# Kernel tuning notes

Hardware: AMD Instinct MI355X
Metric: run time of the kernel (lower is better)

## Reference

```python
import jax, jax.numpy as jnp
import numpy as np

DIM = 768
NUM_HEADS = 12
WH, WW = 14, 14
N_TOK = WH * WW + 1  # 197, includes CLS token
NUM_REL_DIST = (2 * WH - 1) * (2 * WW - 1) + 3  # 732
HEAD_DIM = DIM // NUM_HEADS
SCALE = HEAD_DIM ** -0.5


def _relative_position_index():
    # Mirrors the torch buffer construction (constant, int).
    coords = np.stack(np.meshgrid(np.arange(WH), np.arange(WW), indexing='ij'))  # [2,WH,WW]
    cf = coords.reshape(2, -1)  # [2, WH*WW]
    rel = cf[:, :, None] - cf[:, None, :]  # [2, N, N]
    rel = rel.transpose(1, 2, 0).astype(np.int64)
    rel[:, :, 0] += WH - 1
    rel[:, :, 1] += WW - 1
    rel[:, :, 0] *= 2 * WW - 1
    idx = np.zeros((N_TOK, N_TOK), dtype=np.int64)
    idx[1:, 1:] = rel.sum(-1)
    idx[0, 0:] = NUM_REL_DIST - 3
    idx[0:, 0] = NUM_REL_DIST - 2
    idx[0, 0] = NUM_REL_DIST - 1
    return jnp.asarray(idx)

REL_POS_INDEX = _relative_position_index()


def setup_inputs() -> dict:
    key = jax.random.key(0)
    ks = jax.random.split(key, 7)
    B = 64
    x = jax.random.normal(ks[0], (B, N_TOK, DIM), dtype=jnp.float32)
    qkv_weight = jax.random.normal(ks[1], (3 * DIM, DIM), dtype=jnp.float32) * 0.02
    q_bias = jax.random.normal(ks[2], (DIM,), dtype=jnp.float32) * 0.02
    v_bias = jax.random.normal(ks[3], (DIM,), dtype=jnp.float32) * 0.02
    rel_pos_bias_table = jax.random.normal(ks[4], (NUM_REL_DIST, NUM_HEADS), dtype=jnp.float32) * 0.02
    proj_weight = jax.random.normal(ks[5], (DIM, DIM), dtype=jnp.float32) * 0.02
    proj_bias = jax.random.normal(ks[6], (DIM,), dtype=jnp.float32) * 0.02
    return {"x": x, "qkv_weight": qkv_weight, "q_bias": q_bias, "v_bias": v_bias,
            "rel_pos_bias_table": rel_pos_bias_table, "proj_weight": proj_weight,
            "proj_bias": proj_bias}


def reference(x, qkv_weight, q_bias, v_bias, rel_pos_bias_table, proj_weight, proj_bias):
    B, N, C = x.shape
    qkv_bias = jnp.concatenate([q_bias, jnp.zeros_like(v_bias), v_bias])
    qkv = x @ qkv_weight.T + qkv_bias  # [B, N, 3C]
    qkv = qkv.reshape(B, N, 3, NUM_HEADS, HEAD_DIM).transpose(2, 0, 3, 1, 4)
    q, k, v = qkv[0], qkv[1], qkv[2]  # each [B, H, N, D]
    attn = jnp.einsum('bhnd,bhmd->bhnm', q * SCALE, k)  # [B, H, N, N]
    rpb = rel_pos_bias_table[REL_POS_INDEX]  # [N, N, H]
    attn = attn + rpb.transpose(2, 0, 1)[None]  # [1, H, N, N]
    attn = jax.nn.softmax(attn, axis=-1)
    out = jnp.einsum('bhnm,bhmd->bhnd', attn, v)  # [B, H, N, D]
    out = out.transpose(0, 2, 1, 3).reshape(B, N, C)
    return out @ proj_weight.T + proj_bias
```

## Files before the change

### kernel.cpp

```cpp
#include <hip/hip_runtime.h>
#include <hip/hip_bf16.h>

#define DIM 768
#define NHEADS 12
#define NTOK 197
#define NP 208
#define NPS 232
#define M_ROWS 12608
#define M_PAD 12672
#define HEADS_TOT 768

typedef __attribute__((ext_vector_type(8))) short bf16x8;
typedef __attribute__((ext_vector_type(4))) float f32x4;

__device__ inline short f2bf(float f) {
  union { __hip_bfloat16 h; short s; } u;
  u.h = __float2bfloat16(f);
  return u.s;
}

__device__ __forceinline__ void gload16(const short* g, short* l) {
  __builtin_amdgcn_global_load_lds((const __attribute__((address_space(1))) void*)g,
                                   (__attribute__((address_space(3))) void*)l, 16, 0, 0);
}

__device__ __forceinline__ int xcd_swz(int orig, int nwg) {
  int q = nwg >> 3, r = nwg & 7;
  int x = orig & 7, p = orig >> 3;
  return (x < r ? x * (q + 1) : r * (q + 1) + (x - r) * q) + p;
}

__global__ void convert_kernel(const float* __restrict__ x, const float* __restrict__ wq,
                               const float* __restrict__ wp,
                               short* __restrict__ xb, short* __restrict__ wqb,
                               short* __restrict__ wpb) {
  int idx = blockIdx.x * 256 + threadIdx.x;
  const int n_x  = M_ROWS * DIM / 4;
  const int n_wq = 3 * DIM * DIM / 4;
  const int n_wp = DIM * DIM / 4;
  const float4* src; short* dst; int off;
  if (idx < n_x)                { src = (const float4*)x;  dst = xb;  off = idx; }
  else if (idx < n_x + n_wq)    { src = (const float4*)wq; dst = wqb; off = idx - n_x; }
  else if (idx < n_x + n_wq + n_wp) { src = (const float4*)wp; dst = wpb; off = idx - n_x - n_wq; }
  else return;
  float4 v = src[off];
  short4 o;
  o.x = f2bf(v.x); o.y = f2bf(v.y); o.z = f2bf(v.z); o.w = f2bf(v.w);
  *(short4*)(dst + (size_t)off * 4) = o;
}

__global__ void rpb_kernel(const float* __restrict__ table, float* __restrict__ rpbf) {
  int idx = blockIdx.x * 256 + threadIdx.x;
  const int tot = NHEADS * NP * NP;
  if (idx >= tot) return;
  int h = idx / (NP * NP);
  int rem = idx - h * NP * NP;
  int i = rem / NP;
  int j = rem - i * NP;
  float v = 0.f;
  if (i < NTOK && j < NTOK) {
    int t;
    if (i == 0 && j == 0) t = 731;
    else if (i == 0)      t = 729;
    else if (j == 0)      t = 730;
    else {
      int p = i - 1, q = j - 1;
      int ri = p / 14, ci = p - ri * 14;
      int rj = q / 14, cj = q - rj * 14;
      t = (ri - rj + 13) * 27 + (ci - cj + 13);
    }
    v = table[t * NHEADS + h];
  }
  rpbf[idx] = v;
}

__device__ inline void gemm_tile_mainloop(const short* __restrict__ A, const short* __restrict__ Bw,
                                          int tm, int tn,
                                          short* As0, short* Bs0, short* As1, short* Bs1,
                                          f32x4 (&acc)[4][4]) {
  const int tid = threadIdx.x;
  const int l = tid & 63, lr = l & 15, lg = l >> 4;
  const int w = tid >> 6, wm = w >> 1, wn = w & 1;
  const int row = tid >> 2;
  const int c8 = (((tid & 3) ^ ((tid >> 3) & 3)) << 3);
  const int rs = (((lg ^ ((lr >> 1) & 3))) << 3);
  const short* Ag = A + (size_t)(tm * 128 + row) * DIM + c8;
  const short* Bg = Bw + (size_t)(tn * 128 + row) * DIM + c8;
  const int dOff = tid * 8;
#pragma unroll
  for (int m = 0; m < 4; ++m)
#pragma unroll
    for (int n = 0; n < 4; ++n) { f32x4 z = {0.f, 0.f, 0.f, 0.f}; acc[m][n] = z; }

  gload16(Ag, As0 + dOff);
  gload16(Ag + (size_t)64 * DIM, As0 + 2048 + dOff);
  gload16(Bg, Bs0 + dOff);
  gload16(Bg + (size_t)64 * DIM, Bs0 + 2048 + dOff);
  __syncthreads();

  const int NT = DIM / 32;
  for (int kt = 0; kt < NT; ++kt) {
    short* Ac = (kt & 1) ? As1 : As0;
    short* Bc = (kt & 1) ? Bs1 : Bs0;
    short* An = (kt & 1) ? As0 : As1;
    short* Bn = (kt & 1) ? Bs0 : Bs1;
    if (kt < NT - 1) {
      gload16(Ag + (kt + 1) * 32, An + dOff);
      gload16(Ag + (size_t)64 * DIM + (kt + 1) * 32, An + 2048 + dOff);
      gload16(Bg + (kt + 1) * 32, Bn + dOff);
      gload16(Bg + (size_t)64 * DIM + (kt + 1) * 32, Bn + 2048 + dOff);
    }
    bf16x8 af[4], bfr[4];
#pragma unroll
    for (int m = 0; m < 4; ++m)
      af[m] = *(const bf16x8*)(Ac + (wm * 64 + m * 16 + lr) * 32 + rs);
#pragma unroll
    for (int n = 0; n < 4; ++n)
      bfr[n] = *(const bf16x8*)(Bc + (wn * 64 + n * 16 + lr) * 32 + rs);
#pragma unroll
    for (int m = 0; m < 4; ++m)
#pragma unroll
      for (int n = 0; n < 4; ++n)
        acc[m][n] = __builtin_amdgcn_mfma_f32_16x16x32_bf16(af[m], bfr[n], acc[m][n], 0, 0, 0);
    __syncthreads();
  }
}

__global__ void gemm_qkv_kernel(const short* __restrict__ xb, const short* __restrict__ wqb,
                                const float* __restrict__ q_bias, const float* __restrict__ v_bias,
                                short* __restrict__ qbuf, short* __restrict__ kbuf,
                                short* __restrict__ vtbuf) {
  __shared__ __attribute__((aligned(16))) short As0[128 * 32];
  __shared__ __attribute__((aligned(16))) short Bs0[128 * 32];
  __shared__ __attribute__((aligned(16))) short As1[128 * 32];
  __shared__ __attribute__((aligned(16))) short Bs1[128 * 32];
  const int wg = xcd_swz(blockIdx.x, 99 * 18);
  const int tn = wg % 18, tm = wg / 18;
  f32x4 acc[4][4];
  gemm_tile_mainloop(xb, wqb, tm, tn, As0, Bs0, As1, Bs1, acc);

  const int tid = threadIdx.x;
  const int w = tid >> 6, l = tid & 63, lr = l & 15, lg = l >> 4;
  const int wm = w >> 1, wn = w & 1;
  const int rbase = tm * 128 + wm * 64, cbase = tn * 128 + wn * 64;
#pragma unroll
  for (int n = 0; n < 4; ++n) {
    int c = cbase + n * 16 + lr;
    int part = (c < 768) ? 0 : ((c < 1536) ? 1 : 2);
    int f = c - part * 768;
    int hh = f >> 6, d = f & 63;
    float bias = (part == 0) ? q_bias[c] : ((part == 2) ? v_bias[f] : 0.f);
#pragma unroll
    for (int m = 0; m < 4; ++m) {
#pragma unroll
      for (int i = 0; i < 4; ++i) {
        int r = rbase + m * 16 + lg * 4 + i;
        if (r < M_ROWS) {
          int b = r / 197, nn = r - b * 197;
          int bh = b * 12 + hh;
          float v = acc[m][n][i] + bias;
          if (part == 0)      qbuf[(size_t)(bh * NP + nn) * 64 + d] = f2bf(v * 0.125f);
          else if (part == 1) kbuf[(size_t)(bh * NP + nn) * 64 + d] = f2bf(v);
          else                vtbuf[(size_t)(bh * 64 + d) * NP + nn] = f2bf(v);
        }
      }
    }
  }
}

__global__ __launch_bounds__(512, 1)
void attn_kernel(const short* __restrict__ qbuf, const short* __restrict__ kbuf,
                 const short* __restrict__ vtbuf, const float* __restrict__ rpbf,
                 short* __restrict__ aout) {
  __shared__ __attribute__((aligned(16))) short Klds[208 * 64];
  __shared__ __attribute__((aligned(16))) short Vlds[64 * NPS];
  __shared__ __attribute__((aligned(16))) short Plds[8 * 16 * NPS];
  const int bh = blockIdx.x;
  const int b = bh / 12, h = bh - b * 12;
  const short* Qg = qbuf + (size_t)bh * NP * 64;
  const short* Kg = kbuf + (size_t)bh * NP * 64;
  const short* Vg = vtbuf + (size_t)bh * 64 * NP;
  const float* RP = rpbf + (size_t)h * NP * NP;
  const int tid = threadIdx.x;
  const int wave = tid >> 6, l = tid & 63, lr = l & 15, lg = l >> 4;

  for (int c = tid; c < 1664; c += 512) {
    int r = c >> 3, sp = c & 7;
    gload16(Kg + r * 64 + ((sp ^ (r & 7)) << 3), Klds + c * 8);
  }
  for (int c = tid; c < 64 * 29; c += 512) {
    int r = c / 29, sp = c - r * 29;
    int sg = sp < 26 ? sp : 25;
    gload16(Vg + r * NP + sg * 8, Vlds + c * 8);
  }
  __syncthreads();
  if (tid < 64) {
    for (int j = NTOK; j < NPS; ++j) Vlds[tid * NPS + j] = 0;
  }
  __syncthreads();

  short* Pw = Plds + wave * 16 * NPS;
  for (int s = wave; s < 13; s += 8) {
    const int row0 = s * 16;
    bf16x8 qf0 = *(const bf16x8*)(Qg + (row0 + lr) * 64 + lg * 8);
    bf16x8 qf1 = *(const bf16x8*)(Qg + (row0 + lr) * 64 + 32 + lg * 8);
    f32x4 acc[13];
#pragma unroll
    for (int t = 0; t < 13; ++t) { f32x4 z = {0.f, 0.f, 0.f, 0.f}; acc[t] = z; }
    __builtin_amdgcn_s_setprio(1);
#pragma unroll
    for (int t = 0; t < 13; ++t) {
      int rk = t * 16 + lr;
      int sw = lr & 7;
      bf16x8 kf0 = *(const bf16x8*)(Klds + rk * 64 + ((lg ^ sw) << 3));
      bf16x8 kf1 = *(const bf16x8*)(Klds + rk * 64 + (((4 + lg) ^ sw) << 3));
      acc[t] = __builtin_amdgcn_mfma_f32_16x16x32_bf16(qf0, kf0, acc[t], 0, 0, 0);
      acc[t] = __builtin_amdgcn_mfma_f32_16x16x32_bf16(qf1, kf1, acc[t], 0, 0, 0);
    }
    __builtin_amdgcn_s_setprio(0);
    float sum4[4];
#pragma unroll
    for (int i = 0; i < 4; ++i) {
      const int row = row0 + lg * 4 + i;
      const float* rp = RP + (size_t)row * NP;
      float sv[13];
      float mx = -3e38f;
#pragma unroll
      for (int t = 0; t < 13; ++t) {
        int col = t * 16 + lr;
        float s_ = (col < NTOK) ? (acc[t][i] + rp[col]) : -3e38f;
        sv[t] = s_;
        mx = fmaxf(mx, s_);
      }
      mx = fmaxf(mx, __shfl_xor(mx, 1, 16));
      mx = fmaxf(mx, __shfl_xor(mx, 2, 16));
      mx = fmaxf(mx, __shfl_xor(mx, 4, 16));
      mx = fmaxf(mx, __shfl_xor(mx, 8, 16));
      float sm = 0.f;
#pragma unroll
      for (int t = 0; t < 13; ++t) {
        float p = __expf(sv[t] - mx);
        sm += p;
        Pw[(lg * 4 + i) * NPS + t * 16 + lr] = f2bf(p);
      }
      sm += __shfl_xor(sm, 1, 16);
      sm += __shfl_xor(sm, 2, 16);
      sm += __shfl_xor(sm, 4, 16);
      sm += __shfl_xor(sm, 8, 16);
      sum4[i] = sm;
      Pw[(lg * 4 + i) * NPS + 208 + lr] = 0;
    }
    f32x4 o[4];
#pragma unroll
    for (int dt = 0; dt < 4; ++dt) { f32x4 z = {0.f, 0.f, 0.f, 0.f}; o[dt] = z; }
    __builtin_amdgcn_s_setprio(1);
#pragma unroll
    for (int jb = 0; jb < 7; ++jb) {
      bf16x8 pf = *(const bf16x8*)(Pw + lr * NPS + jb * 32 + lg * 8);
#pragma unroll
      for (int dt = 0; dt < 4; ++dt) {
        bf16x8 vf = *(const bf16x8*)(Vlds + (dt * 16 + lr) * NPS + jb * 32 + lg * 8);
        o[dt] = __builtin_amdgcn_mfma_f32_16x16x32_bf16(pf, vf, o[dt], 0, 0, 0);
      }
    }
    __builtin_amdgcn_s_setprio(0);
#pragma unroll
    for (int i = 0; i < 4; ++i) {
      const int row = row0 + lg * 4 + i;
      if (row < NTOK) {
        float inv = 1.f / sum4[i];
        size_t base = (size_t)(b * 197 + row) * DIM + h * 64;
#pragma unroll
        for (int dt = 0; dt < 4; ++dt)
          aout[base + dt * 16 + lr] = f2bf(o[dt][i] * inv);
      }
    }
  }
}

__global__ void gemm_proj_kernel(const short* __restrict__ ab, const short* __restrict__ wpb,
                                 const float* __restrict__ proj_bias, float* __restrict__ out) {
  __shared__ __attribute__((aligned(16))) short As0[128 * 32];
  __shared__ __attribute__((aligned(16))) short Bs0[128 * 32];
  __shared__ __attribute__((aligned(16))) short As1[128 * 32];
  __shared__ __attribute__((aligned(16))) short Bs1[128 * 32];
  const int wg = xcd_swz(blockIdx.x, 99 * 6);
  const int tn = wg % 6, tm = wg / 6;
  f32x4 acc[4][4];
  gemm_tile_mainloop(ab, wpb, tm, tn, As0, Bs0, As1, Bs1, acc);

  const int tid = threadIdx.x;
  const int w = tid >> 6, l = tid & 63, lr = l & 15, lg = l >> 4;
  const int wm = w >> 1, wn = w & 1;
  const int rbase = tm * 128 + wm * 64, cbase = tn * 128 + wn * 64;
#pragma unroll
  for (int n = 0; n < 4; ++n) {
    int c = cbase + n * 16 + lr;
    float pb = proj_bias[c];
#pragma unroll
    for (int m = 0; m < 4; ++m) {
#pragma unroll
      for (int i = 0; i < 4; ++i) {
        int r = rbase + m * 16 + lg * 4 + i;
        if (r < M_ROWS) out[(size_t)r * DIM + c] = acc[m][n][i] + pb;
      }
    }
  }
}

extern "C" void kernel_launch(void* const* d_in, const int* in_sizes, int n_in,
                              void* d_out, int out_size, void* d_ws, size_t ws_size,
                              hipStream_t stream) {
  const float* x         = (const float*)d_in[0];
  const float* wqkv      = (const float*)d_in[1];
  const float* q_bias    = (const float*)d_in[2];
  const float* v_bias    = (const float*)d_in[3];
  const float* table     = (const float*)d_in[4];
  const float* wproj     = (const float*)d_in[5];
  const float* proj_bias = (const float*)d_in[6];
  float* out = (float*)d_out;

  char* p = (char*)d_ws;
  short* xb    = (short*)p; p += (size_t)M_PAD * DIM * 2;
  short* wqb   = (short*)p; p += (size_t)3 * DIM * DIM * 2;
  short* wpb   = (short*)p; p += (size_t)DIM * DIM * 2;
  short* qbuf  = (short*)p; p += (size_t)HEADS_TOT * NP * 64 * 2;
  short* kbuf  = (short*)p; p += (size_t)HEADS_TOT * NP * 64 * 2;
  short* vtbuf = (short*)p; p += (size_t)HEADS_TOT * 64 * NP * 2;
  float* rpbf  = (float*)p; p += (size_t)NHEADS * NP * NP * 4;
  short* aout  = xb;

  const int conv_tot = (M_ROWS * DIM + 3 * DIM * DIM + DIM * DIM) / 4;
  convert_kernel<<<(conv_tot + 255) / 256, 256, 0, stream>>>(x, wqkv, wproj, xb, wqb, wpb);
  rpb_kernel<<<(NHEADS * NP * NP + 255) / 256, 256, 0, stream>>>(table, rpbf);
  gemm_qkv_kernel<<<99 * 18, 256, 0, stream>>>(xb, wqb, q_bias, v_bias, qbuf, kbuf, vtbuf);
  attn_kernel<<<HEADS_TOT, 512, 0, stream>>>(qbuf, kbuf, vtbuf, rpbf, aout);
  gemm_proj_kernel<<<99 * 6, 256, 0, stream>>>(aout, wpb, proj_bias, out);
}
```

Before: 173.6 us.

## Store QKV as row-major token buffer and gather per-head in attention

The QKV GEMM epilogue now writes a plain row-major [M, 2304] bf16 buffer instead of scattering into per-head Q/K and transposed V buffers, which removes the per-element division and the strided transposed V stores. The attention kernel then reads Q, K and V with a 2304-element row stride, clamping padded rows. V is transposed into LDS with scalar 2-byte loads instead of the 16-byte async copies used before. The input padding grows to 12800 rows and is zeroed in the convert kernel so the extra GEMM tile row reads defined data. The cost moves from scattered global writes in the GEMM to uncoalesced scalar V reads in attention.

```diff
diff --git a/kernel.cpp b/kernel.cpp
--- a/kernel.cpp
+++ b/kernel.cpp
@@ -2,13 +2,15 @@
 #include <hip/hip_bf16.h>
 
 #define DIM 768
+#define QKVD 2304
 #define NHEADS 12
 #define NTOK 197
 #define NP 208
 #define NPS 232
 #define M_ROWS 12608
-#define M_PAD 12672
+#define M_PAD 12800
 #define HEADS_TOT 768
+#define NT 24
 
 typedef __attribute__((ext_vector_type(8))) short bf16x8;
 typedef __attribute__((ext_vector_type(4))) float f32x4;
@@ -38,11 +40,19 @@
   const int n_x  = M_ROWS * DIM / 4;
   const int n_wq = 3 * DIM * DIM / 4;
   const int n_wp = DIM * DIM / 4;
+  const int n_pad = (M_PAD - M_ROWS) * DIM / 4;
+  if (idx >= n_x + n_wq + n_wp) {
+    int k = idx - n_x - n_wq - n_wp;
+    if (k < n_pad) {
+      short4 z = {0, 0, 0, 0};
+      *(short4*)(xb + (size_t)M_ROWS * DIM + (size_t)k * 4) = z;
+    }
+    return;
+  }
   const float4* src; short* dst; int off;
-  if (idx < n_x)                { src = (const float4*)x;  dst = xb;  off = idx; }
-  else if (idx < n_x + n_wq)    { src = (const float4*)wq; dst = wqb; off = idx - n_x; }
-  else if (idx < n_x + n_wq + n_wp) { src = (const float4*)wp; dst = wpb; off = idx - n_x - n_wq; }
-  else return;
+  if (idx < n_x)             { src = (const float4*)x;  dst = xb;  off = idx; }
+  else if (idx < n_x + n_wq) { src = (const float4*)wq; dst = wqb; off = idx - n_x; }
+  else                       { src = (const float4*)wp; dst = wpb; off = idx - n_x - n_wq; }
   float4 v = src[off];
   short4 o;
   o.x = f2bf(v.x); o.y = f2bf(v.y); o.z = f2bf(v.z); o.w = f2bf(v.w);
@@ -74,10 +84,10 @@
   rpbf[idx] = v;
 }
 
-__device__ inline void gemm_tile_mainloop(const short* __restrict__ A, const short* __restrict__ Bw,
-                                          int tm, int tn,
-                                          short* As0, short* Bs0, short* As1, short* Bs1,
-                                          f32x4 (&acc)[4][4]) {
+__device__ inline void gemm_tile_mainloop128(const short* __restrict__ A, const short* __restrict__ Bw,
+                                             int tm, int tn,
+                                             short* As0, short* Bs0, short* As1, short* Bs1,
+                                             f32x4 (&acc)[4][4]) {
   const int tid = threadIdx.x;
   const int l = tid & 63, lr = l & 15, lg = l >> 4;
   const int w = tid >> 6, wm = w >> 1, wn = w & 1;
@@ -98,7 +108,6 @@
   gload16(Bg + (size_t)64 * DIM, Bs0 + 2048 + dOff);
   __syncthreads();
 
-  const int NT = DIM / 32;
   for (int kt = 0; kt < NT; ++kt) {
     short* Ac = (kt & 1) ? As1 : As0;
     short* Bc = (kt & 1) ? Bs1 : Bs0;
@@ -128,16 +137,15 @@
 
 __global__ void gemm_qkv_kernel(const short* __restrict__ xb, const short* __restrict__ wqb,
                                 const float* __restrict__ q_bias, const float* __restrict__ v_bias,
-                                short* __restrict__ qbuf, short* __restrict__ kbuf,
-                                short* __restrict__ vtbuf) {
+                                short* __restrict__ qkvb) {
   __shared__ __attribute__((aligned(16))) short As0[128 * 32];
   __shared__ __attribute__((aligned(16))) short Bs0[128 * 32];
   __shared__ __attribute__((aligned(16))) short As1[128 * 32];
   __shared__ __attribute__((aligned(16))) short Bs1[128 * 32];
-  const int wg = xcd_swz(blockIdx.x, 99 * 18);
+  const int wg = xcd_swz(blockIdx.x, 100 * 18);
   const int tn = wg % 18, tm = wg / 18;
   f32x4 acc[4][4];
-  gemm_tile_mainloop(xb, wqb, tm, tn, As0, Bs0, As1, Bs1, acc);
+  gemm_tile_mainloop128(xb, wqb, tm, tn, As0, Bs0, As1, Bs1, acc);
 
   const int tid = threadIdx.x;
   const int w = tid >> 6, l = tid & 63, lr = l & 15, lg = l >> 4;
@@ -147,63 +155,57 @@
   for (int n = 0; n < 4; ++n) {
     int c = cbase + n * 16 + lr;
     int part = (c < 768) ? 0 : ((c < 1536) ? 1 : 2);
-    int f = c - part * 768;
-    int hh = f >> 6, d = f & 63;
-    float bias = (part == 0) ? q_bias[c] : ((part == 2) ? v_bias[f] : 0.f);
+    float bias = (part == 0) ? q_bias[c] : ((part == 2) ? v_bias[c - 1536] : 0.f);
+    float scl = (part == 0) ? 0.125f : 1.f;
 #pragma unroll
     for (int m = 0; m < 4; ++m) {
 #pragma unroll
       for (int i = 0; i < 4; ++i) {
         int r = rbase + m * 16 + lg * 4 + i;
-        if (r < M_ROWS) {
-          int b = r / 197, nn = r - b * 197;
-          int bh = b * 12 + hh;
-          float v = acc[m][n][i] + bias;
-          if (part == 0)      qbuf[(size_t)(bh * NP + nn) * 64 + d] = f2bf(v * 0.125f);
-          else if (part == 1) kbuf[(size_t)(bh * NP + nn) * 64 + d] = f2bf(v);
-          else                vtbuf[(size_t)(bh * 64 + d) * NP + nn] = f2bf(v);
-        }
+        qkvb[(size_t)r * QKVD + c] = f2bf((acc[m][n][i] + bias) * scl);
       }
     }
   }
 }
 
 __global__ __launch_bounds__(512, 1)
-void attn_kernel(const short* __restrict__ qbuf, const short* __restrict__ kbuf,
-                 const short* __restrict__ vtbuf, const float* __restrict__ rpbf,
+void attn_kernel(const short* __restrict__ qkvb, const float* __restrict__ rpbf,
                  short* __restrict__ aout) {
   __shared__ __attribute__((aligned(16))) short Klds[208 * 64];
   __shared__ __attribute__((aligned(16))) short Vlds[64 * NPS];
   __shared__ __attribute__((aligned(16))) short Plds[8 * 16 * NPS];
   const int bh = blockIdx.x;
   const int b = bh / 12, h = bh - b * 12;
-  const short* Qg = qbuf + (size_t)bh * NP * 64;
-  const short* Kg = kbuf + (size_t)bh * NP * 64;
-  const short* Vg = vtbuf + (size_t)bh * 64 * NP;
+  const short* base = qkvb + (size_t)(b * 197) * QKVD;
+  const short* Qg = base + h * 64;
+  const short* Kg = base + 768 + h * 64;
+  const short* Vg = base + 1536 + h * 64;
   const float* RP = rpbf + (size_t)h * NP * NP;
   const int tid = threadIdx.x;
   const int wave = tid >> 6, l = tid & 63, lr = l & 15, lg = l >> 4;
 
   for (int c = tid; c < 1664; c += 512) {
     int r = c >> 3, sp = c & 7;
-    gload16(Kg + r * 64 + ((sp ^ (r & 7)) << 3), Klds + c * 8);
-  }
-  for (int c = tid; c < 64 * 29; c += 512) {
-    int r = c / 29, sp = c - r * 29;
-    int sg = sp < 26 ? sp : 25;
-    gload16(Vg + r * NP + sg * 8, Vlds + c * 8);
+    int rr = r < NTOK ? r : NTOK - 1;
+    gload16(Kg + (size_t)rr * QKVD + ((sp ^ (r & 7)) << 3), Klds + c * 8);
+  }
+  for (int idx = tid; idx < 64 * NP; idx += 512) {
+    int t = idx >> 6, d = idx & 63;
+    int tt = t < NTOK ? t : NTOK - 1;
+    Vlds[d * NPS + t] = Vg[(size_t)tt * QKVD + d];
   }
   __syncthreads();
   if (tid < 64) {
-    for (int j = NTOK; j < NPS; ++j) Vlds[tid * NPS + j] = 0;
+    for (int j = NP; j < NPS; ++j) Vlds[tid * NPS + j] = 0;
   }
   __syncthreads();
 
   short* Pw = Plds + wave * 16 * NPS;
   for (int s = wave; s < 13; s += 8) {
     const int row0 = s * 16;
-    bf16x8 qf0 = *(const bf16x8*)(Qg + (row0 + lr) * 64 + lg * 8);
-    bf16x8 qf1 = *(const bf16x8*)(Qg + (row0 + lr) * 64 + 32 + lg * 8);
+    const int qrow = (row0 + lr < NTOK) ? (row0 + lr) : (NTOK - 1);
+    bf16x8 qf0 = *(const bf16x8*)(Qg + (size_t)qrow * QKVD + lg * 8);
+    bf16x8 qf1 = *(const bf16x8*)(Qg + (size_t)qrow * QKVD + 32 + lg * 8);
     f32x4 acc[13];
 #pragma unroll
     for (int t = 0; t < 13; ++t) { f32x4 z = {0.f, 0.f, 0.f, 0.f}; acc[t] = z; }
@@ -269,10 +271,10 @@
       const int row = row0 + lg * 4 + i;
       if (row < NTOK) {
         float inv = 1.f / sum4[i];
-        size_t base = (size_t)(b * 197 + row) * DIM + h * 64;
+        size_t base2 = (size_t)(b * 197 + row) * DIM + h * 64;
 #pragma unroll
         for (int dt = 0; dt < 4; ++dt)
-          aout[base + dt * 16 + lr] = f2bf(o[dt][i] * inv);
+          aout[base2 + dt * 16 + lr] = f2bf(o[dt][i] * inv);
       }
     }
   }
@@ -287,7 +289,7 @@
   const int wg = xcd_swz(blockIdx.x, 99 * 6);
   const int tn = wg % 6, tm = wg / 6;
   f32x4 acc[4][4];
-  gemm_tile_mainloop(ab, wpb, tm, tn, As0, Bs0, As1, Bs1, acc);
+  gemm_tile_mainloop128(ab, wpb, tm, tn, As0, Bs0, As1, Bs1, acc);
 
   const int tid = threadIdx.x;
   const int w = tid >> 6, l = tid & 63, lr = l & 15, lg = l >> 4;
@@ -324,16 +326,14 @@
   short* xb    = (short*)p; p += (size_t)M_PAD * DIM * 2;
   short* wqb   = (short*)p; p += (size_t)3 * DIM * DIM * 2;
   short* wpb   = (short*)p; p += (size_t)DIM * DIM * 2;
-  short* qbuf  = (short*)p; p += (size_t)HEADS_TOT * NP * 64 * 2;
-  short* kbuf  = (short*)p; p += (size_t)HEADS_TOT * NP * 64 * 2;
-  short* vtbuf = (short*)p; p += (size_t)HEADS_TOT * 64 * NP * 2;
+  short* qkvb  = (short*)p; p += (size_t)M_PAD * QKVD * 2;
   float* rpbf  = (float*)p; p += (size_t)NHEADS * NP * NP * 4;
   short* aout  = xb;
 
-  const int conv_tot = (M_ROWS * DIM + 3 * DIM * DIM + DIM * DIM) / 4;
+  const int conv_tot = (M_ROWS * DIM + 3 * DIM * DIM + DIM * DIM + (M_PAD - M_ROWS) * DIM) / 4;
   convert_kernel<<<(conv_tot + 255) / 256, 256, 0, stream>>>(x, wqkv, wproj, xb, wqb, wpb);
   rpb_kernel<<<(NHEADS * NP * NP + 255) / 256, 256, 0, stream>>>(table, rpbf);
-  gemm_qkv_kernel<<<99 * 18, 256, 0, stream>>>(xb, wqb, q_bias, v_bias, qbuf, kbuf, vtbuf);
-  attn_kernel<<<HEADS_TOT, 512, 0, stream>>>(qbuf, kbuf, vtbuf, rpbf, aout);
+  gemm_qkv_kernel<<<100 * 18, 256, 0, stream>>>(xb, wqb, q_bias, v_bias, qkvb);
+  attn_kernel<<<HEADS_TOT, 512, 0, stream>>>(qkvb, rpbf, aout);
   gemm_proj_kernel<<<99 * 6, 256, 0, stream>>>(aout, wpb, proj_bias, out);
 }
```

After: 159.0 us. -8.4%, faster.
